# Kernel tuning notes

Hardware: AMD Instinct MI355X
Metric: run time of the kernel (lower is better)

Reference implementation:

```python
import jax, jax.numpy as jnp
import numpy as np

B, S, D, H = 2, 2048, 1024, 16
HD = D // H  # 64

def _make_freqs():
    # flux-style rotation matrices: [1,1,S,HD//2,2,2]
    theta = 10000.0
    inv = 1.0 / (theta ** (np.arange(0, HD, 2, dtype=np.float32) / HD))  # [HD//2]
    pos = np.arange(S, dtype=np.float32)
    ang = pos[:, None] * inv[None, :]  # [S, HD//2]
    cos, sin = np.cos(ang), np.sin(ang)
    rot = np.stack([np.stack([cos, -sin], -1), np.stack([sin, cos], -1)], -2)  # [S,HD//2,2,2]
    return jnp.asarray(rot[None, None], dtype=jnp.float32)

def setup_inputs() -> dict:
    key = jax.random.key(0)
    ks = jax.random.split(key, 9)
    sc = 1.0 / np.sqrt(D)
    return {
        "x": jax.random.normal(ks[0], (B, S, D), jnp.float32),
        "freqs": _make_freqs(),
        "Wq": jax.random.normal(ks[1], (D, D), jnp.float32) * sc,
        "bq": jax.random.normal(ks[2], (D,), jnp.float32) * 0.01,
        "Wk": jax.random.normal(ks[3], (D, D), jnp.float32) * sc,
        "bk": jax.random.normal(ks[4], (D,), jnp.float32) * 0.01,
        "Wv": jax.random.normal(ks[5], (D, D), jnp.float32) * sc,
        "bv": jax.random.normal(ks[6], (D,), jnp.float32) * 0.01,
        "Wo": jax.random.normal(ks[7], (D, D), jnp.float32) * sc,
        "bo": jax.random.normal(ks[8], (D,), jnp.float32) * 0.01,
    }

def _apply_rope(xq, xk, freqs):
    # xq/xk: [B,H,S,HD]; freqs: [1,1,S,HD//2,2,2]
    def rot(t):
        t_ = t.reshape(*t.shape[:-1], -1, 1, 2)  # [B,H,S,HD//2,1,2]
        out = freqs[..., 0] * t_[..., 0] + freqs[..., 1] * t_[..., 1]  # [B,H,S,HD//2,2]
        return out.reshape(t.shape).astype(t.dtype)
    return rot(xq), rot(xk)

def reference(x, freqs, Wq, bq, Wk, bk, Wv, bv, Wo, bo):
    b, s, _ = x.shape
    # QKV projections (torch Linear: x @ W.T + b)
    q = (x @ Wq.T + bq).reshape(b, s, H, HD).transpose(0, 2, 1, 3)  # [B,H,S,HD]
    k = (x @ Wk.T + bk).reshape(b, s, H, HD).transpose(0, 2, 1, 3)
    v = (x @ Wv.T + bv).reshape(b, s, H, HD).transpose(0, 2, 1, 3)
    q, k = _apply_rope(q, k, freqs)
    # scaled dot product attention, no mask, no dropout
    scale = 1.0 / jnp.sqrt(jnp.asarray(HD, x.dtype))
    scores = jnp.einsum("bhqd,bhkd->bhqk", q, k) * scale
    attn = jax.nn.softmax(scores, axis=-1)
    o = jnp.einsum("bhqk,bhkd->bhqd", attn, v)  # [B,H,S,HD]
    o = o.transpose(0, 2, 1, 3).reshape(b, s, D)
    return o @ Wo.T + bo
```

## Files before the change

### kernel.cpp

```cpp
#include <hip/hip_runtime.h>
#include <cmath>

#define B_ 2
#define S_ 2048
#define D_ 1024
#define H_ 16
#define HD_ 64
#define M_ 4096

typedef __attribute__((ext_vector_type(8))) short short8;
typedef __attribute__((ext_vector_type(4))) short short4v;
typedef __attribute__((ext_vector_type(4))) float f32x4;

__device__ __forceinline__ short f2bf(float x) {
    unsigned u = __builtin_bit_cast(unsigned, x);
    u += 0x7fffu + ((u >> 16) & 1u);
    return (short)(u >> 16);
}

__device__ __forceinline__ void gload_lds16(const short* g, short* l) {
    __builtin_amdgcn_global_load_lds(
        (const __attribute__((address_space(1))) unsigned int*)g,
        (__attribute__((address_space(3))) unsigned int*)l, 16, 0, 0);
}

template<int N> __device__ __forceinline__ void vwait() {
    if constexpr (N == 0) asm volatile("s_waitcnt vmcnt(0)" ::: "memory");
    else if constexpr (N == 2) asm volatile("s_waitcnt vmcnt(2)" ::: "memory");
    else if constexpr (N == 3) asm volatile("s_waitcnt vmcnt(3)" ::: "memory");
    else if constexpr (N == 4) asm volatile("s_waitcnt vmcnt(4)" ::: "memory");
}
__device__ __forceinline__ void bar() { __builtin_amdgcn_s_barrier(); }

__global__ __launch_bounds__(256) void cast_all_kernel(
    const float* __restrict__ x,  const float* __restrict__ Wq,
    const float* __restrict__ Wk, const float* __restrict__ Wv,
    const float* __restrict__ Wo,
    short* __restrict__ xb, short* __restrict__ Wqkvb, short* __restrict__ Wob)
{
    const size_t i = (size_t)blockIdx.x * 256 + threadIdx.x;
    const float* src; short* dst; size_t off;
    if (i < 1048576)      { src = x;  dst = xb;              off = i; }
    else if (i < 1310720) { src = Wq; dst = Wqkvb;           off = i - 1048576; }
    else if (i < 1572864) { src = Wk; dst = Wqkvb + 1048576; off = i - 1310720; }
    else if (i < 1835008) { src = Wv; dst = Wqkvb + 2097152; off = i - 1572864; }
    else                  { src = Wo; dst = Wob;             off = i - 1835008; }
    float4 v = ((const float4*)src)[off];
    short4v o = { f2bf(v.x), f2bf(v.y), f2bf(v.z), f2bf(v.w) };
    ((short4v*)dst)[off] = o;
}

__global__ __launch_bounds__(256) void gemm_qkv(
    const short* __restrict__ A, const short* __restrict__ Bw,
    const float* __restrict__ b0p, const float* __restrict__ b1p, const float* __restrict__ b2p,
    const float* __restrict__ freqs,
    short* __restrict__ out0, short* __restrict__ out1, short* __restrict__ out2)
{
    constexpr int TM = 128, TN = 128, RT = 4, CT = 4, LPC = 4;
    __shared__ __align__(16) short A0[TM*32];
    __shared__ __align__(16) short A1[TM*32];
    __shared__ __align__(16) short A2[TM*32];
    __shared__ __align__(16) short B0[TN*32];
    __shared__ __align__(16) short B1[TN*32];
    __shared__ __align__(16) short B2[TN*32];
    const int t = threadIdx.x;
    const int w = t >> 6;
    const int lane = t & 63;
    const int qd = lane >> 4, l = lane & 15;
    const int n0 = blockIdx.x * TN, m0 = blockIdx.y * TM;
    const int wr = (w >> 1) * (TM/2), wc = (w & 1) * (TN/2);
    const int srow  = lane >> 2;
    const int sslot = ((lane & 3) ^ ((lane >> 3) & 3)) * 8;
    const int rsw = (l >> 1) & 3;

    f32x4 acc[RT][CT] = {};

    auto STAGE = [&](int c, short* As, short* Bss) {
        const int k0 = c * 32;
        #pragma unroll
        for (int j = 0; j < TM/64; ++j) {
            const int r0 = (j*4 + w) * 16;
            gload_lds16(A + (size_t)(m0 + r0 + srow)*1024 + k0 + sslot, &As[r0*32]);
        }
        #pragma unroll
        for (int j = 0; j < TN/64; ++j) {
            const int r0 = (j*4 + w) * 16;
            gload_lds16(Bw + (size_t)(n0 + r0 + srow)*1024 + k0 + sslot, &Bss[r0*32]);
        }
    };

    auto COMP = [&](const short* As, const short* Bss) {
        short8 af[RT], bfr[CT];
        #pragma unroll
        for (int rt = 0; rt < RT; ++rt)
            af[rt] = *(const short8*)&As[(wr + rt*16 + l)*32 + ((qd ^ rsw) << 3)];
        #pragma unroll
        for (int ct = 0; ct < CT; ++ct)
            bfr[ct] = *(const short8*)&Bss[(wc + ct*16 + l)*32 + ((qd ^ rsw) << 3)];
        #pragma unroll
        for (int rt = 0; rt < RT; ++rt)
            #pragma unroll
            for (int ct = 0; ct < CT; ++ct)
                acc[rt][ct] = __builtin_amdgcn_mfma_f32_16x16x32_bf16(af[rt], bfr[ct], acc[rt][ct], 0, 0, 0);
    };

    STAGE(0, A0, B0);
    STAGE(1, A1, B1);
    for (int p = 0; p <= 27; p += 3) {
        vwait<LPC>(); bar();
        STAGE(p + 2, A2, B2);
        COMP(A0, B0);
        vwait<LPC>(); bar();
        STAGE(p + 3, A0, B0);
        COMP(A1, B1);
        vwait<LPC>(); bar();
        STAGE(p + 4, A1, B1);
        COMP(A2, B2);
    }
    vwait<LPC>(); bar();
    COMP(A0, B0);
    vwait<0>(); bar();
    COMP(A1, B1);

    const int sel = n0 >> 10;
    const int nb = n0 & 1023;
    const float* bias = (sel == 0) ? b0p : (sel == 1) ? b1p : b2p;
    if (sel < 2) {
        short* outg = (sel == 0) ? out0 : out1;
        #pragma unroll
        for (int rt = 0; rt < RT; ++rt)
            #pragma unroll
            for (int ct = 0; ct < CT; ++ct) {
                const int d = nb + wc + ct*16 + l;
                const float bsv = bias[d];
                const int h = d >> 6, hd = d & 63;
                #pragma unroll
                for (int r = 0; r < 4; ++r) {
                    const int m = m0 + wr + rt*16 + qd*4 + r;
                    const int bb = m >> 11, s = m & 2047;
                    float val = acc[rt][ct][r] + bsv;
                    float pv = __shfl_xor(val, 1);
                    const float* f = freqs + (size_t)s*128 + (size_t)(hd >> 1)*4;
                    float o = (d & 1) ? (f[2]*pv + f[3]*val) : (f[0]*val + f[1]*pv);
                    outg[((size_t)(bb*16 + h)*2048 + s)*64 + hd] = f2bf(o);
                }
            }
    } else {
        #pragma unroll
        for (int rt = 0; rt < RT; ++rt)
            #pragma unroll
            for (int ct = 0; ct < CT; ++ct) {
                const int d = nb + wc + ct*16 + l;
                const float bsv = bias[d];
                const int h = d >> 6, hd = d & 63;
                const int m0r = m0 + wr + rt*16 + qd*4;
                const int bb = m0r >> 11, s0 = m0r & 2047;
                short4v pk;
                #pragma unroll
                for (int r = 0; r < 4; ++r) pk[r] = f2bf(acc[rt][ct][r] + bsv);
                *(short4v*)&out2[((size_t)(bb*16 + h)*64 + hd)*2048 + s0] = pk;
            }
    }
}

__global__ __launch_bounds__(256) void gemm_proj64(
    const short* __restrict__ A, const short* __restrict__ Bw,
    const float* __restrict__ b0p, float* __restrict__ out)
{
    __shared__ __align__(16) short A0[64*64];
    __shared__ __align__(16) short A1[64*64];
    __shared__ __align__(16) short A2[64*64];
    __shared__ __align__(16) short B0[64*64];
    __shared__ __align__(16) short B1[64*64];
    __shared__ __align__(16) short B2[64*64];
    const int t = threadIdx.x;
    const int w = t >> 6;
    const int lane = t & 63;
    const int qd = lane >> 4, l = lane & 15;
    const int l7 = lane & 7;
    const int n0 = blockIdx.x * 64, m0 = blockIdx.y * 64;
    const int wr = (w >> 1) * 32, wc = (w & 1) * 32;
    const int rl  = lane >> 3;
    const int ss8 = ((lane & 7) ^ rl) << 3;

    f32x4 acc[2][2] = {};

    auto STAGE = [&](int c, short* As, short* Bss) {
        const int k0 = c * 64;
        #pragma unroll
        for (int j = 0; j < 2; ++j) {
            const int r0 = (j*4 + w) * 8;
            gload_lds16(A  + (size_t)(m0 + r0 + rl)*1024 + k0 + ss8, &As[r0*64]);
            gload_lds16(Bw + (size_t)(n0 + r0 + rl)*1024 + k0 + ss8, &Bss[r0*64]);
        }
    };

    auto COMP = [&](const short* As, const short* Bss) {
        #pragma unroll
        for (int kk = 0; kk < 2; ++kk) {
            short8 af[2], bfr[2];
            #pragma unroll
            for (int rt = 0; rt < 2; ++rt)
                af[rt] = *(const short8*)&As[(wr + rt*16 + l)*64 + (((kk*4 + qd) ^ l7) << 3)];
            #pragma unroll
            for (int ct = 0; ct < 2; ++ct)
                bfr[ct] = *(const short8*)&Bss[(wc + ct*16 + l)*64 + (((kk*4 + qd) ^ l7) << 3)];
            #pragma unroll
            for (int rt = 0; rt < 2; ++rt)
                #pragma unroll
                for (int ct = 0; ct < 2; ++ct)
                    acc[rt][ct] = __builtin_amdgcn_mfma_f32_16x16x32_bf16(af[rt], bfr[ct], acc[rt][ct], 0, 0, 0);
        }
    };

    STAGE(0, A0, B0);
    STAGE(1, A1, B1);
    for (int p = 0; p <= 9; p += 3) {
        vwait<4>(); bar();
        STAGE(p + 2, A2, B2);
        COMP(A0, B0);
        vwait<4>(); bar();
        STAGE(p + 3, A0, B0);
        COMP(A1, B1);
        vwait<4>(); bar();
        STAGE(p + 4, A1, B1);
        COMP(A2, B2);
    }
    vwait<4>(); bar();
    STAGE(14, A2, B2);
    COMP(A0, B0);
    vwait<4>(); bar();
    STAGE(15, A0, B0);
    COMP(A1, B1);
    vwait<4>(); bar();
    COMP(A2, B2);
    vwait<0>(); bar();
    COMP(A0, B0);

    #pragma unroll
    for (int rt = 0; rt < 2; ++rt)
        #pragma unroll
        for (int ct = 0; ct < 2; ++ct) {
            const int n = n0 + wc + ct*16 + l;
            const float bias = b0p[n];
            #pragma unroll
            for (int r = 0; r < 4; ++r) {
                const int m = m0 + wr + rt*16 + qd*4 + r;
                out[(size_t)m*1024 + n] = acc[rt][ct][r] + bias;
            }
        }
}

__global__ __launch_bounds__(512) void attn_mfma(
    const short* __restrict__ qg, const short* __restrict__ kg,
    const short* __restrict__ vtg, short* __restrict__ og)
{
    __shared__ __align__(16) short Ka[64*64];
    __shared__ __align__(16) short Kb[64*64];
    __shared__ __align__(16) short Kc[64*64];
    __shared__ __align__(16) short Kd[64*64];
    __shared__ __align__(16) short Va[64*64];
    __shared__ __align__(16) short Vb[64*64];
    __shared__ __align__(16) short Vc[64*64];
    __shared__ __align__(16) short Vd[64*64];
    __shared__ __align__(16) short Pb[128*64];

    const int t = threadIdx.x;
    const int w = t >> 6;
    const int lane = t & 63;
    const int qd = lane >> 4, l = lane & 15;
    const int l7 = lane & 7;
    const int q0 = blockIdx.x * 128;
    const int bh = blockIdx.y;

    const int rl  = lane >> 3;
    const int ss8 = ((lane & 7) ^ rl) << 3;

    short8 qf[2];
    const short* qb = qg + ((size_t)bh*2048 + q0 + w*16)*64;
    #pragma unroll
    for (int kf = 0; kf < 2; ++kf)
        qf[kf] = *(const short8*)&qb[l*64 + kf*32 + qd*8];

    f32x4 oacc[4] = {};
    float lsum = 0.f;

    const short* kbase = kg  + (size_t)bh*2048*64;
    const short* vbase = vtg + (size_t)bh*64*2048;
    const float SC = 0.125f * 1.44269504088896340736f;

    auto PREF = [&](int c, short* Kdst, short* Vdst) {
        gload_lds16(kbase + (size_t)(c*64 + w*8 + rl)*64 + ss8,   &Kdst[(w*8)*64]);
        gload_lds16(vbase + (size_t)(w*8 + rl)*2048 + c*64 + ss8, &Vdst[(w*8)*64]);
    };

    auto TILE = [&](const short* Kc_, const short* Vc_) {
        f32x4 sacc[4] = {};
        #pragma unroll
        for (int ct = 0; ct < 4; ++ct) {
            short8 k0f = *(const short8*)&Kc_[(ct*16 + l)*64 + (((0 + qd) ^ l7) << 3)];
            short8 k1f = *(const short8*)&Kc_[(ct*16 + l)*64 + (((4 + qd) ^ l7) << 3)];
            sacc[ct] = __builtin_amdgcn_mfma_f32_16x16x32_bf16(k0f, qf[0], sacc[ct], 0, 0, 0);
            sacc[ct] = __builtin_amdgcn_mfma_f32_16x16x32_bf16(k1f, qf[1], sacc[ct], 0, 0, 0);
        }
        #pragma unroll
        for (int ct = 0; ct < 4; ++ct) {
            float p0 = exp2f(sacc[ct][0] * SC);
            float p1 = exp2f(sacc[ct][1] * SC);
            float p2 = exp2f(sacc[ct][2] * SC);
            float p3 = exp2f(sacc[ct][3] * SC);
            lsum += (p0 + p1) + (p2 + p3);
            union { unsigned u[2]; short4v s; } cv;
            asm("v_cvt_pk_bf16_f32 %0, %1, %2" : "=v"(cv.u[0]) : "v"(p0), "v"(p1));
            asm("v_cvt_pk_bf16_f32 %0, %1, %2" : "=v"(cv.u[1]) : "v"(p2), "v"(p3));
            *(short4v*)&Pb[(w*16 + l)*64 + (((ct*32 + qd*8) ^ (l7 << 4)) >> 1)] = cv.s;
        }
        #pragma unroll
        for (int kf = 0; kf < 2; ++kf) {
            const int so = ((kf*4 + qd) ^ l7) << 3;
            short8 pa = *(const short8*)&Pb[(w*16 + l)*64 + so];
            #pragma unroll
            for (int ht = 0; ht < 4; ++ht) {
                short8 vb = *(const short8*)&Vc_[(ht*16 + l)*64 + so];
                oacc[ht] = __builtin_amdgcn_mfma_f32_16x16x32_bf16(pa, vb, oacc[ht], 0, 0, 0);
            }
        }
    };

    PREF(0, Ka, Va); PREF(1, Kb, Vb);
    for (int P = 0; P < 16; P += 2) {
        vwait<0>(); bar();
        if (P < 15) { PREF(2*P + 2, Kc, Vc); PREF(2*P + 3, Kd, Vd); }
        TILE(Ka, Va); TILE(Kb, Vb);
        vwait<0>(); bar();
        if (P + 2 < 16) { PREF(2*P + 4, Ka, Va); PREF(2*P + 5, Kb, Vb); }
        TILE(Kc, Vc); TILE(Kd, Vd);
    }

    lsum += __shfl_xor(lsum, 16);
    lsum += __shfl_xor(lsum, 32);
    float inv[4];
    #pragma unroll
    for (int r = 0; r < 4; ++r)
        inv[r] = 1.0f / __shfl(lsum, qd*4 + r);

    const int bb = bh >> 4, h = bh & 15;
    #pragma unroll
    for (int ht = 0; ht < 4; ++ht)
        #pragma unroll
        for (int r = 0; r < 4; ++r) {
            const int s = q0 + w*16 + qd*4 + r;
            og[((size_t)bb*2048 + s)*1024 + h*64 + ht*16 + l] =
                f2bf(oacc[ht][r] * inv[r]);
        }
}

extern "C" void kernel_launch(void* const* d_in, const int* in_sizes, int n_in,
                              void* d_out, int out_size, void* d_ws, size_t ws_size,
                              hipStream_t stream)
{
    const float* x  = (const float*)d_in[0];
    const float* fr = (const float*)d_in[1];
    const float* Wq = (const float*)d_in[2];
    const float* bq = (const float*)d_in[3];
    const float* Wk = (const float*)d_in[4];
    const float* bk = (const float*)d_in[5];
    const float* Wv = (const float*)d_in[6];
    const float* bv = (const float*)d_in[7];
    const float* Wo = (const float*)d_in[8];
    const float* bo = (const float*)d_in[9];
    float* out = (float*)d_out;

    short* ws    = (short*)d_ws;
    short* xb    = ws;
    short* Wqkvb = xb    + 4194304;
    short* Wob   = Wqkvb + 3145728;
    short* qg    = Wob   + 1048576;
    short* kg    = qg    + 4194304;
    short* vtg   = kg    + 4194304;
    short* og    = vtg   + 4194304;

    cast_all_kernel<<<8192, 256, 0, stream>>>(x, Wq, Wk, Wv, Wo, xb, Wqkvb, Wob);
    gemm_qkv<<<dim3(24, 32), 256, 0, stream>>>(xb, Wqkvb, bq, bk, bv, fr, qg, kg, vtg);
    attn_mfma<<<dim3(16, 32), 512, 0, stream>>>(qg, kg, vtg, og);
    gemm_proj64<<<dim3(16, 64), 256, 0, stream>>>(og, Wob, bo, out);
}
```

Before: 254.4 us.

## Replace paired double-buffered K/V prefetch with a three-stage rolling pipeline

```diff
diff --git a/kernel.cpp b/kernel.cpp
--- a/kernel.cpp
+++ b/kernel.cpp
@@ -255,14 +255,12 @@
     const short* __restrict__ qg, const short* __restrict__ kg,
     const short* __restrict__ vtg, short* __restrict__ og)
 {
-    __shared__ __align__(16) short Ka[64*64];
-    __shared__ __align__(16) short Kb[64*64];
-    __shared__ __align__(16) short Kc[64*64];
-    __shared__ __align__(16) short Kd[64*64];
-    __shared__ __align__(16) short Va[64*64];
-    __shared__ __align__(16) short Vb[64*64];
-    __shared__ __align__(16) short Vc[64*64];
-    __shared__ __align__(16) short Vd[64*64];
+    __shared__ __align__(16) short K0[64*64];
+    __shared__ __align__(16) short K1[64*64];
+    __shared__ __align__(16) short K2[64*64];
+    __shared__ __align__(16) short V0[64*64];
+    __shared__ __align__(16) short V1[64*64];
+    __shared__ __align__(16) short V2[64*64];
     __shared__ __align__(16) short Pb[128*64];
 
     const int t = threadIdx.x;
@@ -289,17 +287,17 @@
     const short* vbase = vtg + (size_t)bh*64*2048;
     const float SC = 0.125f * 1.44269504088896340736f;
 
-    auto PREF = [&](int c, short* Kdst, short* Vdst) {
-        gload_lds16(kbase + (size_t)(c*64 + w*8 + rl)*64 + ss8,   &Kdst[(w*8)*64]);
-        gload_lds16(vbase + (size_t)(w*8 + rl)*2048 + c*64 + ss8, &Vdst[(w*8)*64]);
-    };
-
-    auto TILE = [&](const short* Kc_, const short* Vc_) {
+    auto PREF = [&](int c, short* Kd, short* Vd) {
+        gload_lds16(kbase + (size_t)(c*64 + w*8 + rl)*64 + ss8,   &Kd[(w*8)*64]);
+        gload_lds16(vbase + (size_t)(w*8 + rl)*2048 + c*64 + ss8, &Vd[(w*8)*64]);
+    };
+
+    auto TILE = [&](const short* Kc, const short* Vc) {
         f32x4 sacc[4] = {};
         #pragma unroll
         for (int ct = 0; ct < 4; ++ct) {
-            short8 k0f = *(const short8*)&Kc_[(ct*16 + l)*64 + (((0 + qd) ^ l7) << 3)];
-            short8 k1f = *(const short8*)&Kc_[(ct*16 + l)*64 + (((4 + qd) ^ l7) << 3)];
+            short8 k0f = *(const short8*)&Kc[(ct*16 + l)*64 + (((0 + qd) ^ l7) << 3)];
+            short8 k1f = *(const short8*)&Kc[(ct*16 + l)*64 + (((4 + qd) ^ l7) << 3)];
             sacc[ct] = __builtin_amdgcn_mfma_f32_16x16x32_bf16(k0f, qf[0], sacc[ct], 0, 0, 0);
             sacc[ct] = __builtin_amdgcn_mfma_f32_16x16x32_bf16(k1f, qf[1], sacc[ct], 0, 0, 0);
         }
@@ -321,21 +319,29 @@
             short8 pa = *(const short8*)&Pb[(w*16 + l)*64 + so];
             #pragma unroll
             for (int ht = 0; ht < 4; ++ht) {
-                short8 vb = *(const short8*)&Vc_[(ht*16 + l)*64 + so];
+                short8 vb = *(const short8*)&Vc[(ht*16 + l)*64 + so];
                 oacc[ht] = __builtin_amdgcn_mfma_f32_16x16x32_bf16(pa, vb, oacc[ht], 0, 0, 0);
             }
         }
     };
 
-    PREF(0, Ka, Va); PREF(1, Kb, Vb);
-    for (int P = 0; P < 16; P += 2) {
-        vwait<0>(); bar();
-        if (P < 15) { PREF(2*P + 2, Kc, Vc); PREF(2*P + 3, Kd, Vd); }
-        TILE(Ka, Va); TILE(Kb, Vb);
-        vwait<0>(); bar();
-        if (P + 2 < 16) { PREF(2*P + 4, Ka, Va); PREF(2*P + 5, Kb, Vb); }
-        TILE(Kc, Vc); TILE(Kd, Vd);
+    PREF(0, K0, V0);
+    PREF(1, K1, V1);
+    for (int p = 0; p <= 27; p += 3) {
+        vwait<2>(); bar();
+        PREF(p + 2, K2, V2);
+        TILE(K0, V0);
+        vwait<2>(); bar();
+        PREF(p + 3, K0, V0);
+        TILE(K1, V1);
+        vwait<2>(); bar();
+        PREF(p + 4, K1, V1);
+        TILE(K2, V2);
     }
+    vwait<2>(); bar();
+    TILE(K0, V0);
+    vwait<0>(); bar();
+    TILE(K1, V1);
 
     lsum += __shfl_xor(lsum, 16);
     lsum += __shfl_xor(lsum, 32);
```

Measured after the change: 240.5 us. 5.5% less time.
